# Kernel tuning notes

Measured on AMD Instinct MI355X. Metric: run time of the kernel, lower is better.

## Reference

```python
import jax, jax.numpy as jnp
import numpy as np

B, S, E, H = 2, 1024, 4096, 16
D = E // H          # head_dim = 256
RD = 64             # rotary_dim
# Quantization scales (alpha of the int8 GEMM epilogues)
A_QKV = 1.2e-4      # W8A8B8O8 q/k/v projection output scale
A_QK = 2e-4         # BMM_S8T_S8N_F32T alpha (= q_scale * k_scale)
A_PV = 1.0 / 127.0  # BMM_S8T_S8N_S8T alpha (probs quantized by *127)
A_O = 0.01          # W8A8BFP32OFP32 out_proj alpha


def setup_inputs() -> dict:
    key = jax.random.key(0)
    ks = jax.random.split(key, 9)
    ri = lambda k, shp: jax.random.randint(k, shp, -127, 128).astype(jnp.float32)
    return {
        "hidden_states": ri(ks[0], (B, S, E)),   # int8-valued activations
        "Wq": ri(ks[1], (E, E)),
        "Wk": ri(ks[2], (E, E)),
        "Wv": ri(ks[3], (E, E)),
        "Wo": ri(ks[4], (E, E)),
        "bq": ri(ks[5], (E,)),
        "bk": ri(ks[6], (E,)),
        "bv": ri(ks[7], (E,)),
        "bo": jax.random.normal(ks[8], (E,), dtype=jnp.float32) * 0.02,  # fp32 bias
    }


def _linear_i8(x, W, b, alpha):
    # W8A8B8O8Linear: int8 GEMM, scaled, +int8 bias, round+saturate to int8
    y = alpha * (x @ W.T) + b
    return jnp.clip(jnp.round(y), -128, 127)


def _rotate_every_two(x):
    x1 = x[..., ::2]
    x2 = x[..., 1::2]
    return jnp.stack((-x2, x1), axis=-1).reshape(x.shape)


def _apply_rotary(x, sin, cos):
    # duplicate_interleave == repeat each column twice; broadcast over [B, S, H, rd]
    sin = jnp.repeat(sin, 2, axis=-1)[None, :, None, :]
    cos = jnp.repeat(cos, 2, axis=-1)[None, :, None, :]
    r = x * cos + _rotate_every_two(x) * sin
    # torch: clamp(-128,127).to(int8) -> truncate toward zero
    return jnp.trunc(jnp.clip(r, -128.0, 127.0))


def reference(hidden_states, Wq, Wk, Wv, Wo, bq, bk, bv, bo):
    q = _linear_i8(hidden_states, Wq, bq, A_QKV).reshape(B, S, H, D)
    k = _linear_i8(hidden_states, Wk, bk, A_QKV).reshape(B, S, H, D)
    v = _linear_i8(hidden_states, Wv, bv, A_QKV).reshape(B, S, H, D)
    v = v.transpose(0, 2, 1, 3)  # [B, H, S, D]

    # fixed_pos_embedding over rotary_dim
    inv_freq = 1.0 / (10000.0 ** (jnp.arange(0, RD, 2, dtype=jnp.float32) / RD))
    t = jnp.arange(S, dtype=jnp.float32)
    sinusoid = t[:, None] * inv_freq[None, :]   # [S, RD/2]
    sin, cos = jnp.sin(sinusoid), jnp.cos(sinusoid)

    q = jnp.concatenate([_apply_rotary(q[..., :RD], sin, cos), q[..., RD:]], axis=-1)
    k = jnp.concatenate([_apply_rotary(k[..., :RD], sin, cos), k[..., RD:]], axis=-1)
    q = q.transpose(0, 2, 1, 3)  # [B, H, S, D]
    k = k.transpose(0, 2, 1, 3)

    w = A_QK * jnp.einsum('bhqd,bhkd->bhqk', q, k)
    causal = jnp.tril(jnp.ones((S, S), dtype=bool))[None, None]
    w = jnp.where(causal, w, jnp.finfo(jnp.float32).min)
    w = w / jnp.sqrt(jnp.float32(D))  # scale_attn = sqrt(head_dim)
    p = jnp.round(jax.nn.softmax(w, axis=-1) * 127.0)  # int8-valued probs

    # pv_bmm: int8 probs x int8 values -> scaled, round+saturate to int8
    o = jnp.clip(jnp.round(A_PV * jnp.einsum('bhqk,bhkd->bhqd', p, v)), -128, 127)
    o = o.transpose(0, 2, 1, 3).reshape(B, S, E)  # merge heads

    # out_proj: W8A8BFP32OFP32 -> fp32 output
    return A_O * (o @ Wo.T) + bo
```

## Files before the change

kernel.cpp:

```cpp
#include <hip/hip_runtime.h>
#include <hip/hip_bf16.h>

typedef int int32x4 __attribute__((ext_vector_type(4)));
typedef signed char i8;

#define B_ 2
#define S_ 1024
#define E_ 4096
#define H_ 16
#define D_ 256

#define MFMA_I8(a, b, c) __builtin_amdgcn_mfma_i32_16x16x64_i8((a), (b), (c), 0, 0, 0)

__device__ __forceinline__ int32x4 ld16(const void* p) {
    return *reinterpret_cast<const int32x4*>(p);
}

__device__ __forceinline__ void gload16(const void* g, void* l) {
    __builtin_amdgcn_global_load_lds(
        (const __attribute__((address_space(1))) void*)g,
        (__attribute__((address_space(3))) void*)l, 16, 0, 0);
}

#define WAIT_VM3()  asm volatile("s_waitcnt vmcnt(3)" ::: "memory")
#define WAIT_VM0()  asm volatile("s_waitcnt vmcnt(0)" ::: "memory")
#define COMPILER_FENCE() asm volatile("" ::: "memory")

__device__ __forceinline__ int pack4(float4 f) {
    union { int w; i8 b[4]; } u;
    u.b[0] = (i8)f.x; u.b[1] = (i8)f.y; u.b[2] = (i8)f.z; u.b[3] = (i8)f.w;
    return u.w;
}

__global__ void k_f32_to_i8(const float* __restrict__ src, i8* __restrict__ dst, int n4) {
    int i = blockIdx.x * blockDim.x + threadIdx.x;
    if (i >= n4) return;
    reinterpret_cast<int*>(dst)[i] = pack4(reinterpret_cast<const float4*>(src)[i]);
}

__global__ void k_w_to_i8(const float* __restrict__ w0, const float* __restrict__ w1,
                          const float* __restrict__ w2, const float* __restrict__ w3,
                          i8* __restrict__ d0, i8* __restrict__ d1,
                          i8* __restrict__ d2, i8* __restrict__ d3, int n4) {
    int i = blockIdx.x * blockDim.x + threadIdx.x;
    if (i >= n4) return;
    const float* src = (blockIdx.y == 0) ? w0 : (blockIdx.y == 1) ? w1 : (blockIdx.y == 2) ? w2 : w3;
    i8* dst = (blockIdx.y == 0) ? d0 : (blockIdx.y == 1) ? d1 : (blockIdx.y == 2) ? d2 : d3;
    reinterpret_cast<int*>(dst)[i] = pack4(reinterpret_cast<const float4*>(src)[i]);
}

__global__ void k_sincos(float* __restrict__ sin_t, float* __restrict__ cos_t) {
    int idx = blockIdx.x * blockDim.x + threadIdx.x;
    if (idx >= S_ * 32) return;
    int s = idx >> 5, i = idx & 31;
    float ex = (float)(2 * i) / 64.0f;
    float invf = 1.0f / powf(10000.0f, ex);
    float arg = (float)s * invf;
    sin_t[idx] = (float)sin((double)arg);
    cos_t[idx] = (float)cos((double)arg);
}

template<bool OUT_I8>
__device__ __forceinline__ void gemm_core(
    const i8* __restrict__ X, const i8* __restrict__ W, const float* __restrict__ bias,
    void* __restrict__ out, float alpha, int M, int N, int K, i8* lds)
{
    const int nt = K >> 6;
    const int nwg = (M >> 8) * (N >> 7);
    const int q = nwg >> 3;
    const int lin = blockIdx.x;
    const int wg = (lin & 7) * q + (lin >> 3);
    const int nbm = M >> 8;
    const int m0 = (wg % nbm) * 256, n0 = (wg / nbm) * 128;

    const int tid = threadIdx.x, lane = tid & 63, wave = tid >> 6;
    const int wr = wave >> 1, wc = wave & 1, l4 = lane & 15, lh = lane >> 4;

    const int g4 = lh ^ ((l4 >> 1) & 3);
    const int aoff = (wr * 64 + l4) * 64 + g4 * 16;
    const int boff = 16384 + (wc * 64 + l4) * 64 + g4 * 16;

    const int srow = tid >> 2;
    const int sg = (tid & 3) ^ ((tid >> 3) & 3);
    const i8* Asrc = X + (size_t)(m0 + srow) * K + sg * 16;
    const i8* Bsrc = W + (size_t)(n0 + srow) * K + sg * 16;
    const size_t rstep = (size_t)128 * K;
    const int ldst = wave * 1024;

#define BUF3(t_) (lds + ((t_) % 3) * 24576)
#define STAGE3(t_) do { int kb_ = (t_) * 64; i8* lb_ = BUF3(t_);             \
        gload16(Asrc + kb_,         lb_ + ldst);                             \
        gload16(Asrc + rstep + kb_, lb_ + 8192 + ldst);                      \
        gload16(Bsrc + kb_,         lb_ + 16384 + ldst); } while (0)

    int32x4 acc[4][4];
#pragma unroll
    for (int m = 0; m < 4; ++m)
#pragma unroll
        for (int n = 0; n < 4; ++n) acc[m][n] = int32x4{0, 0, 0, 0};

    STAGE3(0);
    STAGE3(1);

    for (int t = 0; t < nt; ++t) {
        const i8* Tb = BUF3(t);
        if (t + 1 < nt) { WAIT_VM3(); } else { WAIT_VM0(); }
        __builtin_amdgcn_s_barrier();
        COMPILER_FENCE();

        if (t + 2 < nt) STAGE3(t + 2);

        int32x4 a0, a1, a2, a3, b0, b1, b2, b3;
        a0 = ld16(Tb + aoff);
        b0 = ld16(Tb + boff);        b1 = ld16(Tb + boff + 1024);
        b2 = ld16(Tb + boff + 2048); b3 = ld16(Tb + boff + 3072);
        a1 = ld16(Tb + aoff + 1024);
        a2 = ld16(Tb + aoff + 2048); a3 = ld16(Tb + aoff + 3072);
        __builtin_amdgcn_s_setprio(1);
        acc[0][0] = MFMA_I8(a0, b0, acc[0][0]);
        acc[0][1] = MFMA_I8(a0, b1, acc[0][1]);
        acc[0][2] = MFMA_I8(a0, b2, acc[0][2]);
        acc[0][3] = MFMA_I8(a0, b3, acc[0][3]);
        acc[1][0] = MFMA_I8(a1, b0, acc[1][0]);
        acc[1][1] = MFMA_I8(a1, b1, acc[1][1]);
        acc[1][2] = MFMA_I8(a1, b2, acc[1][2]);
        acc[1][3] = MFMA_I8(a1, b3, acc[1][3]);
        acc[2][0] = MFMA_I8(a2, b0, acc[2][0]);
        acc[2][1] = MFMA_I8(a2, b1, acc[2][1]);
        acc[2][2] = MFMA_I8(a2, b2, acc[2][2]);
        acc[2][3] = MFMA_I8(a2, b3, acc[2][3]);
        acc[3][0] = MFMA_I8(a3, b0, acc[3][0]);
        acc[3][1] = MFMA_I8(a3, b1, acc[3][1]);
        acc[3][2] = MFMA_I8(a3, b2, acc[3][2]);
        acc[3][3] = MFMA_I8(a3, b3, acc[3][3]);
        __builtin_amdgcn_s_setprio(0);
    }
#undef BUF3
#undef STAGE3

#pragma unroll
    for (int m = 0; m < 4; ++m)
#pragma unroll
        for (int n = 0; n < 4; ++n)
#pragma unroll
            for (int r = 0; r < 4; ++r) {
                int grow = m0 + wr * 64 + m * 16 + lh * 4 + r;
                int gcol = n0 + wc * 64 + n * 16 + l4;
                float y = alpha * (float)acc[m][n][r] + bias[gcol];
                if (OUT_I8) {
                    float v = rintf(y);
                    v = fminf(fmaxf(v, -128.0f), 127.0f);
                    reinterpret_cast<i8*>(out)[(size_t)grow * N + gcol] = (i8)v;
                } else {
                    reinterpret_cast<float*>(out)[(size_t)grow * N + gcol] = y;
                }
            }
}

__global__ __launch_bounds__(512, 4) void k_gemm_qkv(
    const i8* __restrict__ X,
    const i8* __restrict__ w0, const i8* __restrict__ w1, const i8* __restrict__ w2,
    const float* __restrict__ b0, const float* __restrict__ b1, const float* __restrict__ b2,
    i8* __restrict__ o0, i8* __restrict__ o1, i8* __restrict__ o2,
    float alpha, int M, int N, int K)
{
    __shared__ __align__(16) i8 lds[3 * 24576];
    int z = blockIdx.z;
    const i8* W = (z == 0) ? w0 : (z == 1) ? w1 : w2;
    const float* bias = (z == 0) ? b0 : (z == 1) ? b1 : b2;
    i8* out = (z == 0) ? o0 : (z == 1) ? o1 : o2;
    gemm_core<true>(X, W, bias, out, alpha, M, N, K, lds);
}

__global__ __launch_bounds__(512, 4) void k_gemm_out(
    const i8* __restrict__ X, const i8* __restrict__ W, const float* __restrict__ bias,
    float* __restrict__ out, float alpha, int M, int N, int K)
{
    __shared__ __align__(16) i8 lds[3 * 24576];
    gemm_core<false>(X, W, bias, out, alpha, M, N, K, lds);
}

__global__ void k_rope(const i8* __restrict__ qin, const i8* __restrict__ kin,
                       i8* __restrict__ qout, i8* __restrict__ kout,
                       const float* __restrict__ sin_t, const float* __restrict__ cos_t)
{
    const i8* in = blockIdx.y ? kin : qin;
    i8* outp = blockIdx.y ? kout : qout;
    int t = threadIdx.x;
    int row = blockIdx.x * 16 + (t >> 4);
    int seg = t & 15;
    int b = row >> 14;
    int s = (row >> 4) & 1023;
    int h = row & 15;
    union { int32x4 v; i8 b8[16]; } u;
    u.v = ld16(in + (size_t)row * D_ + seg * 16);
    if (seg < 4) {
#pragma unroll
        for (int j = 0; j < 16; j += 2) {
            int i = (seg * 16 + j) >> 1;
            float c = cos_t[s * 32 + i], sn = sin_t[s * 32 + i];
            float f1 = (float)u.b8[j], f2 = (float)u.b8[j + 1];
            float r0 = __fadd_rn(__fmul_rn(f1, c), __fmul_rn(-f2, sn));
            float r1 = __fadd_rn(__fmul_rn(f2, c), __fmul_rn(f1, sn));
            u.b8[j]     = (i8)truncf(fminf(fmaxf(r0, -128.0f), 127.0f));
            u.b8[j + 1] = (i8)truncf(fminf(fmaxf(r1, -128.0f), 127.0f));
        }
    }
    *reinterpret_cast<int32x4*>(
        outp + ((size_t)(b * H_ + h) * S_ + s) * D_ + seg * 16) = u.v;
}

__global__ void k_vtrans(const i8* __restrict__ vin, i8* __restrict__ vout) {
    __shared__ int tile[64][17];
    int bh = blockIdx.z;
    int b = bh >> 4, h = bh & 15;
    int s0 = blockIdx.x * 64, d0 = blockIdx.y * 64;
    int t = threadIdx.x;
    {
        int sr = t >> 2, dq = (t & 3) * 16;
        int32x4 v = ld16(vin + ((size_t)(b * S_ + s0 + sr) * H_ + h) * D_ + d0 + dq);
#pragma unroll
        for (int j = 0; j < 4; ++j) tile[sr][dq / 4 + j] = v[j];
    }
    __syncthreads();
    {
        int dr = t >> 2, sq = (t & 3) * 16;
        union { int32x4 v; i8 b[16]; } u;
        const i8* tb = reinterpret_cast<const i8*>(tile);
#pragma unroll
        for (int j = 0; j < 16; ++j) u.b[j] = tb[(sq + j) * 68 + dr];
        *reinterpret_cast<int32x4*>(vout + ((size_t)bh * D_ + d0 + dr) * S_ + s0 + sq) = u.v;
    }
}

struct AttnShared {
    float slx[4][32];
    float r127[32];
    __align__(16) i8 plds[32][80];
};

__device__ __forceinline__ void attn_chunk(int qc, int bh, int tid,
    const i8* __restrict__ Qh, const i8* __restrict__ Kb, const i8* __restrict__ Vb,
    i8* __restrict__ O, AttnShared& sh)
{
    const float C2 = 1.25e-5f * 1.44269504088896f;
    const float APV = 1.0f / 127.0f;
    const int lane = tid & 63, wave = tid >> 6;
    const int l4 = lane & 15, lh = lane >> 4;
    const i8* Qb = Qh + (size_t)(qc * 32) * D_;
    const int nt = (qc * 32 + 31) / 64 + 1;

    int32x4 aq[2][4];
#pragma unroll
    for (int m = 0; m < 2; ++m)
#pragma unroll
        for (int kk = 0; kk < 4; ++kk)
            aq[m][kk] = ld16(Qb + (size_t)(m * 16 + l4) * D_ + kk * 64 + lh * 16);

    float sum_[2][4];
#pragma unroll
    for (int m = 0; m < 2; ++m)
#pragma unroll
        for (int r = 0; r < 4; ++r) sum_[m][r] = 0.0f;

    for (int kt = 0; kt < nt; ++kt) {
        int cb = kt * 64 + wave * 16;
        int32x4 acc0 = int32x4{0,0,0,0}, acc1 = int32x4{0,0,0,0};
#pragma unroll
        for (int kk = 0; kk < 4; ++kk) {
            int32x4 bf = ld16(Kb + (size_t)(cb + l4) * D_ + kk * 64 + lh * 16);
            acc0 = MFMA_I8(aq[0][kk], bf, acc0);
            acc1 = MFMA_I8(aq[1][kk], bf, acc1);
        }
        int gcol = cb + l4;
#pragma unroll
        for (int m = 0; m < 2; ++m) {
            int32x4 accm = m ? acc1 : acc0;
#pragma unroll
            for (int r = 0; r < 4; ++r) {
                int grow = qc * 32 + m * 16 + lh * 4 + r;
                float e = (gcol <= grow) ? exp2f((float)accm[r] * C2) : 0.0f;
                sum_[m][r] += e;
            }
        }
    }

#pragma unroll
    for (int m = 0; m < 2; ++m)
#pragma unroll
        for (int r = 0; r < 4; ++r) {
            float s = sum_[m][r];
            s += __shfl_xor(s, 1);
            s += __shfl_xor(s, 2);
            s += __shfl_xor(s, 4);
            s += __shfl_xor(s, 8);
            if (l4 == 0) sh.slx[wave][m * 16 + lh * 4 + r] = s;
        }
    __syncthreads();
    if (tid < 32)
        sh.r127[tid] = 127.0f /
            (sh.slx[0][tid] + sh.slx[1][tid] + sh.slx[2][tid] + sh.slx[3][tid]);
    __syncthreads();

    int32x4 oacc[2][4];
#pragma unroll
    for (int m = 0; m < 2; ++m)
#pragma unroll
        for (int n = 0; n < 4; ++n) oacc[m][n] = int32x4{0, 0, 0, 0};

    for (int kt = 0; kt < nt; ++kt) {
        int cb = kt * 64 + wave * 16;
        int32x4 acc0 = int32x4{0,0,0,0}, acc1 = int32x4{0,0,0,0};
#pragma unroll
        for (int kk = 0; kk < 4; ++kk) {
            int32x4 bf = ld16(Kb + (size_t)(cb + l4) * D_ + kk * 64 + lh * 16);
            acc0 = MFMA_I8(aq[0][kk], bf, acc0);
            acc1 = MFMA_I8(aq[1][kk], bf, acc1);
        }
        int gcol = cb + l4;
        i8 pv[2][4];
#pragma unroll
        for (int m = 0; m < 2; ++m) {
            int32x4 accm = m ? acc1 : acc0;
#pragma unroll
            for (int r = 0; r < 4; ++r) {
                int rowi = m * 16 + lh * 4 + r;
                int grow = qc * 32 + rowi;
                float e = (gcol <= grow) ? exp2f((float)accm[r] * C2) : 0.0f;
                pv[m][r] = (i8)(int)rintf(e * sh.r127[rowi]);
            }
        }
        __syncthreads();
#pragma unroll
        for (int m = 0; m < 2; ++m)
#pragma unroll
            for (int r = 0; r < 4; ++r)
                sh.plds[m * 16 + lh * 4 + r][wave * 16 + l4] = pv[m][r];
        __syncthreads();
        int32x4 a0 = ld16(&sh.plds[l4][lh * 16]);
        int32x4 a1 = ld16(&sh.plds[16 + l4][lh * 16]);
#pragma unroll
        for (int n = 0; n < 4; ++n) {
            int32x4 bf = ld16(Vb + (size_t)(wave * 64 + n * 16 + l4) * S_ + kt * 64 + lh * 16);
            oacc[0][n] = MFMA_I8(a0, bf, oacc[0][n]);
            oacc[1][n] = MFMA_I8(a1, bf, oacc[1][n]);
        }
    }

    int b = bh >> 4, h = bh & 15;
#pragma unroll
    for (int m = 0; m < 2; ++m)
#pragma unroll
        for (int r = 0; r < 4; ++r) {
            int s = qc * 32 + m * 16 + lh * 4 + r;
#pragma unroll
            for (int n = 0; n < 4; ++n) {
                float o = rintf(APV * (float)oacc[m][n][r]);
                o = fminf(fmaxf(o, -128.0f), 127.0f);
                O[((size_t)(b * S_ + s) * H_ + h) * D_ + wave * 64 + n * 16 + l4] = (i8)o;
            }
        }
}

__global__ __launch_bounds__(256) void k_attn(const i8* __restrict__ Q, const i8* __restrict__ K,
                                              const i8* __restrict__ V, i8* __restrict__ O)
{
    __shared__ AttnShared sh;
    int bh = blockIdx.x;
    int p = blockIdx.y;
    int tid = threadIdx.x;
    const i8* Qh = Q + (size_t)bh * S_ * D_;
    const i8* Kb = K + (size_t)bh * S_ * D_;
    const i8* Vb = V + (size_t)bh * D_ * S_;
    attn_chunk((S_ / 32 - 1) - p, bh, tid, Qh, Kb, Vb, O, sh);
    attn_chunk(p, bh, tid, Qh, Kb, Vb, O, sh);
}

extern "C" void kernel_launch(void* const* d_in, const int* in_sizes, int n_in,
                              void* d_out, int out_size, void* d_ws, size_t ws_size,
                              hipStream_t stream) {
    const float* hs = (const float*)d_in[0];
    const float* Wq = (const float*)d_in[1];
    const float* Wk = (const float*)d_in[2];
    const float* Wv = (const float*)d_in[3];
    const float* Wo = (const float*)d_in[4];
    const float* bq = (const float*)d_in[5];
    const float* bk = (const float*)d_in[6];
    const float* bv = (const float*)d_in[7];
    const float* bo = (const float*)d_in[8];
    float* out = (float*)d_out;

    size_t off = 0;
    char* wsb = (char*)d_ws;
    auto carve = [&](size_t bytes) { char* p = wsb + off; off += (bytes + 255) & ~(size_t)255; return p; };
    const size_t ME = (size_t)B_ * S_ * E_;
    const size_t EE = (size_t)E_ * E_;
    i8* x8  = (i8*)carve(ME);
    i8* wq8 = (i8*)carve(EE);
    i8* wk8 = (i8*)carve(EE);
    i8* wv8 = (i8*)carve(EE);
    i8* wo8 = (i8*)carve(EE);
    i8* q8  = (i8*)carve(ME);
    i8* k8  = (i8*)carve(ME);
    i8* v8  = (i8*)carve(ME);
    i8* qr  = (i8*)carve(ME);
    i8* kr  = (i8*)carve(ME);
    i8* vt  = (i8*)carve(ME);
    i8* o8  = (i8*)carve(ME);
    float* sin_t = (float*)carve((size_t)S_ * 32 * 4);
    float* cos_t = (float*)carve((size_t)S_ * 32 * 4);

    int n4_me = (int)(ME / 4), n4_ee = (int)(EE / 4);
    k_f32_to_i8<<<(n4_me + 255) / 256, 256, 0, stream>>>(hs, x8, n4_me);
    k_w_to_i8<<<dim3((n4_ee + 255) / 256, 4), 256, 0, stream>>>(
        Wq, Wk, Wv, Wo, wq8, wk8, wv8, wo8, n4_ee);
    k_sincos<<<(S_ * 32 + 255) / 256, 256, 0, stream>>>(sin_t, cos_t);

    const int M = B_ * S_, N = E_, Kd = E_;
    const int nwg = (M / 256) * (N / 128);
    k_gemm_qkv<<<dim3(nwg, 1, 3), 512, 0, stream>>>(
        x8, wq8, wk8, wv8, bq, bk, bv, q8, k8, v8, 0.00012f, M, N, Kd);

    k_rope<<<dim3((B_ * S_ * H_) / 16, 2), 256, 0, stream>>>(q8, k8, qr, kr, sin_t, cos_t);
    k_vtrans<<<dim3(S_ / 64, D_ / 64, B_ * H_), 256, 0, stream>>>(v8, vt);
    k_attn<<<dim3(B_ * H_, S_ / 64), 256, 0, stream>>>(qr, kr, vt, o8);

    k_gemm_out<<<nwg, 512, 0, stream>>>(o8, wo8, bo, out, 0.01f, M, N, Kd);
}
```

Baseline: 292.5 us.

## Double-buffer K fragment loads in attention and launch one query chunk per block

The K-fragment global loads in both attention passes are now software-pipelined with two register buffers, so the next tile's loads are issued before the current tile's MFMAs and softmax. The attention grid changes from paired chunks per block (longest plus shortest for load balance) to one 32-row query chunk per block. Blocks are ordered with the heaviest chunks dispatched first. This is meant to hide global load latency and give the scheduler more independent work. In exchange it uses more registers and gives up the explicit pairing that balanced work across blocks.

```diff
diff --git a/kernel.cpp b/kernel.cpp
--- a/kernel.cpp
+++ b/kernel.cpp
@@ -239,6 +239,11 @@
     __align__(16) i8 plds[32][80];
 };
 
+#define LOADK(dst_, kt_) do {                                                 \
+        const i8* kp_ = Kb + (size_t)((kt_) * 64 + wave * 16 + l4) * D_ + lh * 16; \
+        dst_[0] = ld16(kp_);       dst_[1] = ld16(kp_ + 64);                  \
+        dst_[2] = ld16(kp_ + 128); dst_[3] = ld16(kp_ + 192); } while (0)
+
 __device__ __forceinline__ void attn_chunk(int qc, int bh, int tid,
     const i8* __restrict__ Qh, const i8* __restrict__ Kb, const i8* __restrict__ Vb,
     i8* __restrict__ O, AttnShared& sh)
@@ -263,27 +268,41 @@
 #pragma unroll
         for (int r = 0; r < 4; ++r) sum_[m][r] = 0.0f;
 
-    for (int kt = 0; kt < nt; ++kt) {
-        int cb = kt * 64 + wave * 16;
-        int32x4 acc0 = int32x4{0,0,0,0}, acc1 = int32x4{0,0,0,0};
-#pragma unroll
-        for (int kk = 0; kk < 4; ++kk) {
-            int32x4 bf = ld16(Kb + (size_t)(cb + l4) * D_ + kk * 64 + lh * 16);
-            acc0 = MFMA_I8(aq[0][kk], bf, acc0);
-            acc1 = MFMA_I8(aq[1][kk], bf, acc1);
+    int32x4 kA[4], kB[4];
+
+#define BODY_A(kt_, kf_) do {                                                 \
+        int32x4 acc0 = int32x4{0,0,0,0}, acc1 = int32x4{0,0,0,0};             \
+        acc0 = MFMA_I8(aq[0][0], kf_[0], acc0);                               \
+        acc1 = MFMA_I8(aq[1][0], kf_[0], acc1);                               \
+        acc0 = MFMA_I8(aq[0][1], kf_[1], acc0);                               \
+        acc1 = MFMA_I8(aq[1][1], kf_[1], acc1);                               \
+        acc0 = MFMA_I8(aq[0][2], kf_[2], acc0);                               \
+        acc1 = MFMA_I8(aq[1][2], kf_[2], acc1);                               \
+        acc0 = MFMA_I8(aq[0][3], kf_[3], acc0);                               \
+        acc1 = MFMA_I8(aq[1][3], kf_[3], acc1);                               \
+        int gcol = (kt_) * 64 + wave * 16 + l4;                               \
+        _Pragma("unroll")                                                     \
+        for (int m = 0; m < 2; ++m) {                                         \
+            int32x4 accm = m ? acc1 : acc0;                                   \
+            _Pragma("unroll")                                                 \
+            for (int r = 0; r < 4; ++r) {                                     \
+                int grow = qc * 32 + m * 16 + lh * 4 + r;                     \
+                float e = (gcol <= grow) ? exp2f((float)accm[r] * C2) : 0.0f; \
+                sum_[m][r] += e;                                              \
+            }                                                                 \
+        }                                                                     \
+    } while (0)
+
+    LOADK(kA, 0);
+    for (int kt = 0; kt < nt; kt += 2) {
+        if (kt + 1 < nt) LOADK(kB, kt + 1);
+        BODY_A(kt, kA);
+        if (kt + 1 < nt) {
+            if (kt + 2 < nt) LOADK(kA, kt + 2);
+            BODY_A(kt + 1, kB);
         }
-        int gcol = cb + l4;
-#pragma unroll
-        for (int m = 0; m < 2; ++m) {
-            int32x4 accm = m ? acc1 : acc0;
-#pragma unroll
-            for (int r = 0; r < 4; ++r) {
-                int grow = qc * 32 + m * 16 + lh * 4 + r;
-                float e = (gcol <= grow) ? exp2f((float)accm[r] * C2) : 0.0f;
-                sum_[m][r] += e;
-            }
-        }
-    }
+    }
+#undef BODY_A
 
 #pragma unroll
     for (int m = 0; m < 2; ++m)
@@ -308,44 +327,57 @@
 #pragma unroll
         for (int n = 0; n < 4; ++n) oacc[m][n] = int32x4{0, 0, 0, 0};
 
-    for (int kt = 0; kt < nt; ++kt) {
-        int cb = kt * 64 + wave * 16;
-        int32x4 acc0 = int32x4{0,0,0,0}, acc1 = int32x4{0,0,0,0};
-#pragma unroll
-        for (int kk = 0; kk < 4; ++kk) {
-            int32x4 bf = ld16(Kb + (size_t)(cb + l4) * D_ + kk * 64 + lh * 16);
-            acc0 = MFMA_I8(aq[0][kk], bf, acc0);
-            acc1 = MFMA_I8(aq[1][kk], bf, acc1);
+#define BODY_B(kt_, kf_) do {                                                 \
+        int32x4 acc0 = int32x4{0,0,0,0}, acc1 = int32x4{0,0,0,0};             \
+        acc0 = MFMA_I8(aq[0][0], kf_[0], acc0);                               \
+        acc1 = MFMA_I8(aq[1][0], kf_[0], acc1);                               \
+        acc0 = MFMA_I8(aq[0][1], kf_[1], acc0);                               \
+        acc1 = MFMA_I8(aq[1][1], kf_[1], acc1);                               \
+        acc0 = MFMA_I8(aq[0][2], kf_[2], acc0);                               \
+        acc1 = MFMA_I8(aq[1][2], kf_[2], acc1);                               \
+        acc0 = MFMA_I8(aq[0][3], kf_[3], acc0);                               \
+        acc1 = MFMA_I8(aq[1][3], kf_[3], acc1);                               \
+        int gcol = (kt_) * 64 + wave * 16 + l4;                               \
+        i8 pv[2][4];                                                          \
+        _Pragma("unroll")                                                     \
+        for (int m = 0; m < 2; ++m) {                                         \
+            int32x4 accm = m ? acc1 : acc0;                                   \
+            _Pragma("unroll")                                                 \
+            for (int r = 0; r < 4; ++r) {                                     \
+                int rowi = m * 16 + lh * 4 + r;                               \
+                int grow = qc * 32 + rowi;                                    \
+                float e = (gcol <= grow) ? exp2f((float)accm[r] * C2) : 0.0f; \
+                pv[m][r] = (i8)(int)rintf(e * sh.r127[rowi]);                 \
+            }                                                                 \
+        }                                                                     \
+        __syncthreads();                                                      \
+        _Pragma("unroll")                                                     \
+        for (int m = 0; m < 2; ++m)                                           \
+            _Pragma("unroll")                                                 \
+            for (int r = 0; r < 4; ++r)                                       \
+                sh.plds[m * 16 + lh * 4 + r][wave * 16 + l4] = pv[m][r];      \
+        __syncthreads();                                                      \
+        int32x4 a0 = ld16(&sh.plds[l4][lh * 16]);                             \
+        int32x4 a1 = ld16(&sh.plds[16 + l4][lh * 16]);                        \
+        const i8* vp_ = Vb + (size_t)(wave * 64 + l4) * S_ + (kt_) * 64 + lh * 16; \
+        _Pragma("unroll")                                                     \
+        for (int n = 0; n < 4; ++n) {                                         \
+            int32x4 bf = ld16(vp_ + (size_t)(n * 16) * S_);                   \
+            oacc[0][n] = MFMA_I8(a0, bf, oacc[0][n]);                         \
+            oacc[1][n] = MFMA_I8(a1, bf, oacc[1][n]);                         \
+        }                                                                     \
+    } while (0)
+
+    LOADK(kA, 0);
+    for (int kt = 0; kt < nt; kt += 2) {
+        if (kt + 1 < nt) LOADK(kB, kt + 1);
+        BODY_B(kt, kA);
+        if (kt + 1 < nt) {
+            if (kt + 2 < nt) LOADK(kA, kt + 2);
+            BODY_B(kt + 1, kB);
         }
-        int gcol = cb + l4;
-        i8 pv[2][4];
-#pragma unroll
-        for (int m = 0; m < 2; ++m) {
-            int32x4 accm = m ? acc1 : acc0;
-#pragma unroll
-            for (int r = 0; r < 4; ++r) {
-                int rowi = m * 16 + lh * 4 + r;
-                int grow = qc * 32 + rowi;
-                float e = (gcol <= grow) ? exp2f((float)accm[r] * C2) : 0.0f;
-                pv[m][r] = (i8)(int)rintf(e * sh.r127[rowi]);
-            }
-        }
-        __syncthreads();
-#pragma unroll
-        for (int m = 0; m < 2; ++m)
-#pragma unroll
-            for (int r = 0; r < 4; ++r)
-                sh.plds[m * 16 + lh * 4 + r][wave * 16 + l4] = pv[m][r];
-        __syncthreads();
-        int32x4 a0 = ld16(&sh.plds[l4][lh * 16]);
-        int32x4 a1 = ld16(&sh.plds[16 + l4][lh * 16]);
-#pragma unroll
-        for (int n = 0; n < 4; ++n) {
-            int32x4 bf = ld16(Vb + (size_t)(wave * 64 + n * 16 + l4) * S_ + kt * 64 + lh * 16);
-            oacc[0][n] = MFMA_I8(a0, bf, oacc[0][n]);
-            oacc[1][n] = MFMA_I8(a1, bf, oacc[1][n]);
-        }
-    }
+    }
+#undef BODY_B
 
     int b = bh >> 4, h = bh & 15;
 #pragma unroll
@@ -366,14 +398,13 @@
                                               const i8* __restrict__ V, i8* __restrict__ O)
 {
     __shared__ AttnShared sh;
-    int bh = blockIdx.x;
-    int p = blockIdx.y;
+    int bh = blockIdx.y;
+    int qc = (S_ / 32 - 1) - blockIdx.x;
     int tid = threadIdx.x;
     const i8* Qh = Q + (size_t)bh * S_ * D_;
     const i8* Kb = K + (size_t)bh * S_ * D_;
     const i8* Vb = V + (size_t)bh * D_ * S_;
-    attn_chunk((S_ / 32 - 1) - p, bh, tid, Qh, Kb, Vb, O, sh);
-    attn_chunk(p, bh, tid, Qh, Kb, Vb, O, sh);
+    attn_chunk(qc, bh, tid, Qh, Kb, Vb, O, sh);
 }
 
 extern "C" void kernel_launch(void* const* d_in, const int* in_sizes, int n_in,
@@ -423,7 +454,7 @@
 
     k_rope<<<dim3((B_ * S_ * H_) / 16, 2), 256, 0, stream>>>(q8, k8, qr, kr, sin_t, cos_t);
     k_vtrans<<<dim3(S_ / 64, D_ / 64, B_ * H_), 256, 0, stream>>>(v8, vt);
-    k_attn<<<dim3(B_ * H_, S_ / 64), 256, 0, stream>>>(qr, kr, vt, o8);
+    k_attn<<<dim3(S_ / 32, B_ * H_), 256, 0, stream>>>(qr, kr, vt, o8);
 
     k_gemm_out<<<nwg, 512, 0, stream>>>(o8, wo8, bo, out, 0.01f, M, N, Kd);
 }
```

Measured after the change: 325.6 us. +11.4%, slower.
